# Optimization experiments

Hardware: AMD Instinct MI355X
Metric: run time of the kernel (lower is better)

The kernel has to match this reference:

```python
import jax, jax.numpy as jnp
import numpy as np


def setup_inputs() -> dict:
    key = jax.random.key(0)
    k1, k2, k3 = jax.random.split(key, 3)
    x = jax.random.normal(k1, (32, 256, 56, 56), dtype=jnp.float32)
    att_w = jax.random.normal(k2, (4, 256), dtype=jnp.float32) * 0.05  # 1x1 attention conv weight (K, Cin)
    weight = jax.random.normal(k3, (4, 256, 256, 3, 3), dtype=jnp.float32) * 0.05  # (K, Cout, Cin, kh, kw)
    return {"x": x, "att_w": att_w, "weight": weight}


def reference(x, att_w, weight):
    # x: (B, Cin, H, W); att_w: (K, Cin); weight: (K, Cout, Cin, kh, kw)
    # Attention: global avg pool -> 1x1 conv (Cin->K) -> sigmoid  (named softmax_att but is sigmoid)
    pooled = jnp.mean(x, axis=(2, 3))                 # (B, Cin)
    att = jax.nn.sigmoid(pooled @ att_w.T)            # (B, K)
    # Per-sample expert-mixed conv kernels
    agg_w = jnp.einsum('bk,koihw->boihw', att, weight)  # (B, Cout, Cin, kh, kw)

    def conv_one(xi, wi):
        # xi: (Cin, H, W), wi: (Cout, Cin, kh, kw)
        return jax.lax.conv_general_dilated(
            xi[None], wi,
            window_strides=(1, 1),
            padding=[(1, 1), (1, 1)],
            rhs_dilation=(1, 1),
            dimension_numbers=('NCHW', 'OIHW', 'NCHW'),
        )[0]

    out = jax.vmap(conv_one)(x, agg_w)                # (B, Cout, H, W)
    return out
```

## Files before the change

### kernel.cpp

```cpp
#include <hip/hip_runtime.h>

typedef __attribute__((ext_vector_type(8))) short short8;
typedef __attribute__((ext_vector_type(4))) float floatx4;

__device__ __forceinline__ unsigned short bf16_rne(float f) {
  unsigned int u = __builtin_bit_cast(unsigned int, f);
  u += 0x7fffu + ((u >> 16) & 1u);
  return (unsigned short)(u >> 16);
}

__device__ __forceinline__ void glds16(const void* g, void* l) {
  __builtin_amdgcn_global_load_lds((const __attribute__((address_space(1))) void*)g,
                                   (__attribute__((address_space(3))) void*)l, 16, 0, 0);
}


__global__ void zero_pk_kernel(float* __restrict__ pk) {
  pk[threadIdx.x] = 0.f;
}

__global__ __launch_bounds__(256) void prep_kernel(const float* __restrict__ x,
                                                   const float* __restrict__ att_w,
                                                   unsigned short* __restrict__ xpad,
                                                   float* __restrict__ pooledk) {
  const int bid = blockIdx.x;
  const int b   = bid / 196;
  const int rem = bid - b * 196;
  const int cig = rem / 49;
  const int spc = rem - cig * 49;
  const int t  = threadIdx.x;
  const int cs = t >> 6, sl = t & 63;
  const int sp0 = spc * 64;

  __shared__ unsigned short T2[64 * 72];
  __shared__ float red[4][4];

  const float* xrow = x + (size_t)(b * 256 + cig * 64 + cs * 16) * 3136 + sp0 + sl;
  float v[16];
  #pragma unroll
  for (int i = 0; i < 16; ++i) v[i] = xrow[(size_t)i * 3136];

  float acc0 = 0.f, acc1 = 0.f, acc2 = 0.f, acc3 = 0.f;
  #pragma unroll
  for (int i = 0; i < 16; ++i) {
    float s = v[i];
    #pragma unroll
    for (int o = 32; o > 0; o >>= 1) s += __shfl_xor(s, o, 64);
    const int ci = cig * 64 + cs * 16 + i;
    acc0 += s * att_w[0 * 256 + ci];
    acc1 += s * att_w[1 * 256 + ci];
    acc2 += s * att_w[2 * 256 + ci];
    acc3 += s * att_w[3 * 256 + ci];
  }
  if (sl == 0) { red[cs][0] = acc0; red[cs][1] = acc1; red[cs][2] = acc2; red[cs][3] = acc3; }

  short8 w0, w1;
  #pragma unroll
  for (int i = 0; i < 8; ++i) w0[i] = (short)bf16_rne(v[i]);
  #pragma unroll
  for (int i = 0; i < 8; ++i) w1[i] = (short)bf16_rne(v[8 + i]);
  *(short8*)(T2 + sl * 72 + cs * 16) = w0;
  *(short8*)(T2 + sl * 72 + cs * 16 + 8) = w1;
  __syncthreads();

  if (t < 4) {
    float s = red[0][t] + red[1][t] + red[2][t] + red[3][t];
    atomicAdd(&pooledk[b * 4 + t], s);
  }

  unsigned short* xb = xpad + (size_t)b * (8 * 3364 * 32);
  #pragma unroll
  for (int it = 0; it < 2; ++it) {
    const int c = it * 256 + t;
    const int spl = c >> 3, oc8 = c & 7;
    const int cg8 = cig * 8 + oc8;
    const int kc = cg8 >> 2, o2 = cg8 & 3;
    const int spg = sp0 + spl;
    const int h = spg / 56, wc = spg - h * 56;
    const int pos = (h + 1) * 58 + (wc + 1);
    const short8 vv = *(const short8*)(T2 + spl * 72 + oc8 * 8);
    *(short8*)(xb + (size_t)kc * (3364 * 32) + pos * 32 + o2 * 8) = vv;
  }
}

__global__ __launch_bounds__(256) void border_kernel(unsigned short* __restrict__ xpad) {
  const int b = blockIdx.x, quarter = blockIdx.y, t = threadIdx.x;
  const short8 z = {0, 0, 0, 0, 0, 0, 0, 0};
  unsigned short* xb = xpad + (size_t)b * (8 * 3364 * 32);
  for (int it = 0; it < 8; ++it) {
    const int idx = it * 256 + t;
    if (idx >= 1824) break;
    const int s8 = idx & 3, kc = (idx >> 2) & 7, j = idx >> 5;
    const int pi = quarter * 57 + j;
    int h2, w2;
    if (pi < 58)       { h2 = 0;  w2 = pi; }
    else if (pi < 116) { h2 = 57; w2 = pi - 58; }
    else { const int k = pi - 116; h2 = 1 + (k >> 1); w2 = (k & 1) * 57; }
    *(short8*)(xb + (size_t)kc * (3364 * 32) + (h2 * 58 + w2) * 32 + s8 * 8) = z;
  }
}

__global__ void att_kernel(const float* __restrict__ pooledk,
                           float* __restrict__ att) {
  const int t = threadIdx.x;
  const float z = pooledk[t] * (1.f / 3136.f);
  att[t] = 1.f / (1.f + expf(-z));
}

__global__ __launch_bounds__(256) void agg_kernel(const float* __restrict__ w,
                                                  const float* __restrict__ att,
                                                  unsigned short* __restrict__ agg) {
  const int co = blockIdx.x;
  const int t = threadIdx.x;
  __shared__ float W[4][2304];
  __shared__ float attl[128];
  if (t < 128) attl[t] = att[t];
  #pragma unroll
  for (int e = 0; e < 4; ++e) {
    const float* src = w + (size_t)(e * 256 + co) * 2304;
    #pragma unroll
    for (int j = 0; j < 9; ++j) W[e][j * 256 + t] = src[j * 256 + t];
  }
  __syncthreads();

  int widx[9], off9[9];
  #pragma unroll
  for (int j = 0; j < 9; ++j) {
    const int task = j * 256 + t;
    const int cil = task & 31, pair = task >> 5;
    const int kc = pair / 9, rs = pair - kc * 9;
    widx[j] = (kc * 32 + cil) * 9 + rs;
    off9[j] = pair * 8192 + co * 32 + cil;
  }
  for (int b = 0; b < 32; ++b) {
    const float a0 = attl[b * 4 + 0], a1 = attl[b * 4 + 1];
    const float a2 = attl[b * 4 + 2], a3 = attl[b * 4 + 3];
    unsigned short* dst = agg + (size_t)b * 589824;
    #pragma unroll
    for (int j = 0; j < 9; ++j) {
      const int wi = widx[j];
      float s = a0 * W[0][wi] + a1 * W[1][wi] + a2 * W[2][wi] + a3 * W[3][wi];
      dst[off9[j]] = bf16_rne(s);
    }
  }
}

__global__ __launch_bounds__(256) void conv_kernel(const unsigned short* __restrict__ xpad,
                                                   const unsigned short* __restrict__ aggw,
                                                   float* __restrict__ out) {
  __shared__ unsigned short Bsm[348 * 32];
  __shared__ unsigned short Asm[3 * 128 * 32];

  const int t  = threadIdx.x;
  const int bx = blockIdx.x;
  const int p_t  = bx % 25;
  const int co_t = (bx / 25) & 1;
  const int b    = bx / 50;
  const int p0   = p_t * 128;
  const int oh_min = p0 / 56;

  const unsigned short* xb  = xpad + (size_t)b * (8 * 3364 * 32);
  const unsigned short* awb = aggw + (size_t)b * 589824 + co_t * 4096;

  const int lane = t & 63;
  const int wv = t >> 6;
  const int wm = wv >> 1;
  const int wn = wv & 1;
  const int m16 = lane & 15;
  const int q = lane >> 4;

  int aoff[4], boff[4];
  #pragma unroll
  for (int i = 0; i < 4; ++i)
    aoff[i] = (wm * 64 + i * 16 + m16) * 32 + q * 8;
  #pragma unroll
  for (int j = 0; j < 4; ++j) {
    const int pf = p0 + wn * 64 + j * 16 + m16;
    const int oh = pf / 56;
    const int ow = pf - oh * 56;
    boff[j] = ((oh - oh_min) * 58 + ow) * 32 + q * 8;
  }

  floatx4 acc[4][4];
  #pragma unroll
  for (int i = 0; i < 4; ++i)
    #pragma unroll
    for (int j = 0; j < 4; ++j)
      acc[i][j] = (floatx4){0.f, 0.f, 0.f, 0.f};

  for (int kc = 0; kc < 8; ++kc) {
    const unsigned short* xkc = xb + (size_t)kc * (3364 * 32);
    #pragma unroll
    for (int i = 0; i < 6; ++i) {
      const int c = i * 256 + t;
      if (c < 1392) {
        const int pos = c >> 2, sub = c & 3;
        const int prow = pos / 58;
        const int pcol = pos - prow * 58;
        int ih2 = oh_min + prow; if (ih2 > 57) ih2 = 57;
        glds16(xkc + ((size_t)(ih2 * 58 + pcol) * 32 + sub * 8), (void*)(Bsm + c * 8));
      }
    }
    #pragma unroll
    for (int g = 0; g < 3; ++g) {
      #pragma unroll
      for (int i = 0; i < 6; ++i) {
        const int c = i * 256 + t;
        const int rsl = c >> 9;
        const int w5 = c & 511;
        glds16(awb + (size_t)(kc * 9 + g * 3 + rsl) * 8192 + w5 * 8, (void*)(Asm + c * 8));
      }
      __syncthreads();

      #pragma unroll
      for (int rsl = 0; rsl < 3; ++rsl) {
        const int d = (g * 58 + rsl) * 32;
        short8 af[4], bf[4];
        #pragma unroll
        for (int i = 0; i < 4; ++i)
          af[i] = *(const short8*)(Asm + rsl * 4096 + aoff[i]);
        #pragma unroll
        for (int j = 0; j < 4; ++j)
          bf[j] = *(const short8*)(Bsm + boff[j] + d);
        #pragma unroll
        for (int i = 0; i < 4; ++i)
          #pragma unroll
          for (int j = 0; j < 4; ++j)
            acc[i][j] = __builtin_amdgcn_mfma_f32_16x16x32_bf16(af[i], bf[j], acc[i][j], 0, 0, 0);
      }
      __syncthreads();
    }
  }

  #pragma unroll
  for (int i = 0; i < 4; ++i) {
    const int co = co_t * 128 + wm * 64 + i * 16 + q * 4;
    float* orow = out + (size_t)(b * 256 + co) * 3136;
    #pragma unroll
    for (int j = 0; j < 4; ++j) {
      const int pp = p0 + wn * 64 + j * 16 + m16;
      if (pp < 3136) {
        #pragma unroll
        for (int rg = 0; rg < 4; ++rg)
          orow[(size_t)rg * 3136 + pp] = acc[i][j][rg];
      }
    }
  }
}

extern "C" void kernel_launch(void* const* d_in, const int* in_sizes, int n_in,
                              void* d_out, int out_size, void* d_ws, size_t ws_size,
                              hipStream_t stream) {
  const float* x      = (const float*)d_in[0];
  const float* att_w  = (const float*)d_in[1];
  const float* weight = (const float*)d_in[2];
  float* out = (float*)d_out;

  char* ws = (char*)d_ws;
  float* pooledk       = (float*)ws;
  float* att           = (float*)(ws + 32768);
  unsigned short* agg  = (unsigned short*)(ws + 65536);
  unsigned short* xpad = (unsigned short*)(ws + 65536 + 37748736);

  zero_pk_kernel<<<1, 128, 0, stream>>>(pooledk);
  prep_kernel<<<6272, 256, 0, stream>>>(x, att_w, xpad, pooledk);
  border_kernel<<<dim3(32, 4), 256, 0, stream>>>(xpad);
  att_kernel<<<1, 128, 0, stream>>>(pooledk, att);
  agg_kernel<<<256, 256, 0, stream>>>(weight, att, agg);
  conv_kernel<<<1600, 256, 0, stream>>>(xpad, agg, out);
}
```

Measured before the change: 325.3 us.

## Fuse sigmoid into agg kernel, vectorize agg stores, reorder conv blocks

Several changes at once. The pooled-sum reduction in prep now does the weighted accumulation per lane and shuffle-reduces the four accumulators, instead of reducing each of the 16 channels separately. The separate att_kernel launch is removed and the sigmoid is computed inside agg_kernel. agg_kernel is split over 8 batch groups and writes 16-byte short8 vectors instead of scattered 2-byte stores. conv blocks are remapped so consecutive block IDs are spread across batches and tiles, likely for better L2/XCD locality. Each agg block now reloads all four expert weight slices, so weight reads from global memory increase by about eight times.

```diff
diff --git a/kernel.cpp b/kernel.cpp
--- a/kernel.cpp
+++ b/kernel.cpp
@@ -43,14 +43,18 @@
   float acc0 = 0.f, acc1 = 0.f, acc2 = 0.f, acc3 = 0.f;
   #pragma unroll
   for (int i = 0; i < 16; ++i) {
-    float s = v[i];
-    #pragma unroll
-    for (int o = 32; o > 0; o >>= 1) s += __shfl_xor(s, o, 64);
     const int ci = cig * 64 + cs * 16 + i;
-    acc0 += s * att_w[0 * 256 + ci];
-    acc1 += s * att_w[1 * 256 + ci];
-    acc2 += s * att_w[2 * 256 + ci];
-    acc3 += s * att_w[3 * 256 + ci];
+    acc0 += v[i] * att_w[0 * 256 + ci];
+    acc1 += v[i] * att_w[1 * 256 + ci];
+    acc2 += v[i] * att_w[2 * 256 + ci];
+    acc3 += v[i] * att_w[3 * 256 + ci];
+  }
+  #pragma unroll
+  for (int o = 32; o > 0; o >>= 1) {
+    acc0 += __shfl_xor(acc0, o, 64);
+    acc1 += __shfl_xor(acc1, o, 64);
+    acc2 += __shfl_xor(acc2, o, 64);
+    acc3 += __shfl_xor(acc3, o, 64);
   }
   if (sl == 0) { red[cs][0] = acc0; red[cs][1] = acc1; red[cs][2] = acc2; red[cs][3] = acc3; }
 
@@ -100,21 +104,18 @@
   }
 }
 
-__global__ void att_kernel(const float* __restrict__ pooledk,
-                           float* __restrict__ att) {
-  const int t = threadIdx.x;
-  const float z = pooledk[t] * (1.f / 3136.f);
-  att[t] = 1.f / (1.f + expf(-z));
-}
-
 __global__ __launch_bounds__(256) void agg_kernel(const float* __restrict__ w,
-                                                  const float* __restrict__ att,
+                                                  const float* __restrict__ pooledk,
                                                   unsigned short* __restrict__ agg) {
   const int co = blockIdx.x;
+  const int bq = blockIdx.y;
   const int t = threadIdx.x;
   __shared__ float W[4][2304];
-  __shared__ float attl[128];
-  if (t < 128) attl[t] = att[t];
+  __shared__ float attl[16];
+  if (t < 16) {
+    const float z = pooledk[bq * 16 + t] * (1.f / 3136.f);
+    attl[t] = 1.f / (1.f + expf(-z));
+  }
   #pragma unroll
   for (int e = 0; e < 4; ++e) {
     const float* src = w + (size_t)(e * 256 + co) * 2304;
@@ -123,24 +124,35 @@
   }
   __syncthreads();
 
-  int widx[9], off9[9];
-  #pragma unroll
-  for (int j = 0; j < 9; ++j) {
-    const int task = j * 256 + t;
-    const int cil = task & 31, pair = task >> 5;
-    const int kc = pair / 9, rs = pair - kc * 9;
-    widx[j] = (kc * 32 + cil) * 9 + rs;
-    off9[j] = pair * 8192 + co * 32 + cil;
-  }
-  for (int b = 0; b < 32; ++b) {
-    const float a0 = attl[b * 4 + 0], a1 = attl[b * 4 + 1];
-    const float a2 = attl[b * 4 + 2], a3 = attl[b * 4 + 3];
-    unsigned short* dst = agg + (size_t)b * 589824;
-    #pragma unroll
-    for (int j = 0; j < 9; ++j) {
-      const int wi = widx[j];
-      float s = a0 * W[0][wi] + a1 * W[1][wi] + a2 * W[2][wi] + a3 * W[3][wi];
-      dst[off9[j]] = bf16_rne(s);
+  #pragma unroll
+  for (int rep = 0; rep < 2; ++rep) {
+    const int id = rep * 256 + t;
+    if (id < 288) {
+      const int kc  = id / 36;
+      const int rm  = id - kc * 36;
+      const int rs  = rm >> 2;
+      const int oct = rm & 3;
+      const int wib = (kc * 32 + oct * 8) * 9 + rs;
+      const int off = (kc * 9 + rs) * 8192 + co * 32 + oct * 8;
+      float w0[8], w1[8], w2[8], w3[8];
+      #pragma unroll
+      for (int u = 0; u < 8; ++u) {
+        w0[u] = W[0][wib + u * 9];
+        w1[u] = W[1][wib + u * 9];
+        w2[u] = W[2][wib + u * 9];
+        w3[u] = W[3][wib + u * 9];
+      }
+      #pragma unroll
+      for (int bl = 0; bl < 4; ++bl) {
+        const int b = bq * 4 + bl;
+        const float a0 = attl[bl * 4 + 0], a1 = attl[bl * 4 + 1];
+        const float a2 = attl[bl * 4 + 2], a3 = attl[bl * 4 + 3];
+        short8 vv;
+        #pragma unroll
+        for (int u = 0; u < 8; ++u)
+          vv[u] = (short)bf16_rne(a0 * w0[u] + a1 * w1[u] + a2 * w2[u] + a3 * w3[u]);
+        *(short8*)(agg + (size_t)b * 589824 + off) = vv;
+      }
     }
   }
 }
@@ -152,7 +164,8 @@
   __shared__ unsigned short Asm[3 * 128 * 32];
 
   const int t  = threadIdx.x;
-  const int bx = blockIdx.x;
+  const int bx0 = blockIdx.x;
+  const int bx  = (bx0 & 7) * 200 + (bx0 >> 3);
   const int p_t  = bx % 25;
   const int co_t = (bx / 25) & 1;
   const int b    = bx / 50;
@@ -258,14 +271,12 @@
 
   char* ws = (char*)d_ws;
   float* pooledk       = (float*)ws;
-  float* att           = (float*)(ws + 32768);
   unsigned short* agg  = (unsigned short*)(ws + 65536);
   unsigned short* xpad = (unsigned short*)(ws + 65536 + 37748736);
 
   zero_pk_kernel<<<1, 128, 0, stream>>>(pooledk);
   prep_kernel<<<6272, 256, 0, stream>>>(x, att_w, xpad, pooledk);
   border_kernel<<<dim3(32, 4), 256, 0, stream>>>(xpad);
-  att_kernel<<<1, 128, 0, stream>>>(pooledk, att);
-  agg_kernel<<<256, 256, 0, stream>>>(weight, att, agg);
+  agg_kernel<<<dim3(256, 8), 256, 0, stream>>>(weight, pooledk, agg);
   conv_kernel<<<1600, 256, 0, stream>>>(xpad, agg, out);
 }
```

Result: faster. 308.8 us (-5.1%).
